# Kernel tuning notes

Measured on AMD Instinct MI355X. Metric: run time of the kernel, lower is better.

Reference implementation:

```python
import jax, jax.numpy as jnp
import numpy as np

B, T, F, U = 64, 512, 1024, 64


def setup_inputs() -> dict:
    key = jax.random.key(0)
    ks = jax.random.split(key, 6)
    return {
        "x": jax.random.normal(ks[0], (B, T, F), dtype=jnp.float32),
        "kernel": jax.random.normal(ks[1], (F, U), dtype=jnp.float32) * (1.0 / np.sqrt(F)),
        "bias": jax.random.normal(ks[2], (U,), dtype=jnp.float32) * 0.02,
        "chain_kernel": jax.random.normal(ks[3], (U, U), dtype=jnp.float32) * 0.1,
        "left_boundary": jax.random.normal(ks[4], (U,), dtype=jnp.float32) * 0.1,
        "right_boundary": jax.random.normal(ks[5], (U,), dtype=jnp.float32) * 0.1,
    }


def _viterbi_decode(potentials, chain_kernel):
    # potentials: [B, T, U], chain_kernel: [U, U]
    def step(alpha, pot_t):
        # alpha: [B, U] best score ending in each tag at t-1
        scores = alpha[:, :, None] + chain_kernel[None, :, :] + pot_t[:, None, :]  # [B, U_prev, U_cur]
        return jnp.max(scores, axis=1), jnp.argmax(scores, axis=1)

    pots_t = jnp.moveaxis(potentials[:, 1:], 1, 0)  # [T-1, B, U]
    alpha_last, backptrs = jax.lax.scan(step, potentials[:, 0], pots_t)
    last_tag = jnp.argmax(alpha_last, axis=-1)  # [B]

    def back(tag, bp):
        prev = jnp.take_along_axis(bp, tag[:, None], axis=1)[:, 0]
        return prev, prev

    _, tags = jax.lax.scan(back, last_tag, backptrs, reverse=True)  # [T-1, B], positions 0..T-2
    path = jnp.concatenate([jnp.moveaxis(tags, 0, 1), last_tag[:, None]], axis=1)
    return path.astype(jnp.int32)


def reference(x, kernel, bias, chain_kernel, left_boundary, right_boundary):
    # dense projection (activation = linear)
    potentials = jnp.einsum("btf,fu->btu", x, kernel) + bias  # [B, T, U]
    # boundary energies (mask=None path: add to first/last timestep)
    potentials = potentials.at[:, 0, :].add(left_boundary)
    potentials = potentials.at[:, -1, :].add(right_boundary)
    return _viterbi_decode(potentials, chain_kernel)
```

## Files before the change

### kernel.cpp

```cpp
#include <hip/hip_runtime.h>

#define B_ 64
#define T_ 512
#define F_ 1024
#define U_ 64

__global__ __launch_bounds__(256) void crf_gemm_kernel(
    const float* __restrict__ x, const float* __restrict__ w,
    const float* __restrict__ bias, const float* __restrict__ lb,
    const float* __restrict__ rb, float* __restrict__ pot)
{
    const int tid = threadIdx.x;
    const int rt = tid >> 4;
    const int ut = tid & 15;
    const int n0 = blockIdx.x * 128;
    const int r0 = rt * 8;
    const int u0 = ut * 4;

    float acc[8][4];
#pragma unroll
    for (int i = 0; i < 8; ++i)
#pragma unroll
        for (int j = 0; j < 4; ++j) acc[i][j] = 0.f;

    const float* xbase = x + (size_t)(n0 + r0) * F_;

    for (int f4 = 0; f4 < F_ / 4; ++f4) {
        float xv[8][4];
#pragma unroll
        for (int i = 0; i < 8; ++i) {
            const float4 t4 = *reinterpret_cast<const float4*>(
                xbase + (size_t)i * F_ + f4 * 4);
            xv[i][0] = t4.x; xv[i][1] = t4.y; xv[i][2] = t4.z; xv[i][3] = t4.w;
        }
        float kv[4][4];
#pragma unroll
        for (int ff = 0; ff < 4; ++ff) {
            const float4 t4 = *reinterpret_cast<const float4*>(
                w + (size_t)(f4 * 4 + ff) * U_ + u0);
            kv[ff][0] = t4.x; kv[ff][1] = t4.y; kv[ff][2] = t4.z; kv[ff][3] = t4.w;
        }
#pragma unroll
        for (int ff = 0; ff < 4; ++ff)
#pragma unroll
            for (int i = 0; i < 8; ++i)
#pragma unroll
                for (int j = 0; j < 4; ++j)
                    acc[i][j] = fmaf(xv[i][ff], kv[ff][j], acc[i][j]);
    }

    const int t0 = n0 & (T_ - 1);
    const float4 bs4 = *reinterpret_cast<const float4*>(bias + u0);
    const float4 lb4 = *reinterpret_cast<const float4*>(lb + u0);
    const float4 rb4 = *reinterpret_cast<const float4*>(rb + u0);

#pragma unroll
    for (int i = 0; i < 8; ++i) {
        const int n = n0 + r0 + i;
        const int t = t0 + r0 + i;
        float4 o;
        o.x = acc[i][0] + bs4.x;
        o.y = acc[i][1] + bs4.y;
        o.z = acc[i][2] + bs4.z;
        o.w = acc[i][3] + bs4.w;
        if (t == 0)      { o.x += lb4.x; o.y += lb4.y; o.z += lb4.z; o.w += lb4.w; }
        if (t == T_ - 1) { o.x += rb4.x; o.y += rb4.y; o.z += rb4.z; o.w += rb4.w; }
        *reinterpret_cast<float4*>(pot + (size_t)n * U_ + u0) = o;
    }
}

__global__ __launch_bounds__(256) void crf_viterbi_kernel(
    const float* __restrict__ pot, const float* __restrict__ chain,
    int* __restrict__ path)
{
    const int b = blockIdx.x;
    const int tid = threadIdx.x;
    const int u = tid & 63;
    const int g = tid >> 6;

    __shared__ __align__(16) float alpha_s[64];
    __shared__ float pval[4][64];
    __shared__ int   pidx[4][64];
    __shared__ unsigned char bp[T_ - 1][64];

    float chain_r[16];
#pragma unroll
    for (int k = 0; k < 16; ++k)
        chain_r[k] = chain[(size_t)(g * 16 + k) * U_ + u];

    const float* potb = pot + (size_t)b * T_ * U_;

    if (g == 0) alpha_s[u] = potb[u];
    __syncthreads();

    float pc = potb[(size_t)U_ + u];

    for (int t = 1; t < T_; ++t) {
        const int tn = (t + 1 < T_) ? (t + 1) : (T_ - 1);
        const float pn = potb[(size_t)tn * U_ + u];

        const float4* a4 = reinterpret_cast<const float4*>(alpha_s);
        float best = -3.402823466e38f;
        int bidx = 0;
#pragma unroll
        for (int q = 0; q < 4; ++q) {
            const float4 av = a4[g * 4 + q];
            const float avv[4] = {av.x, av.y, av.z, av.w};
#pragma unroll
            for (int kk = 0; kk < 4; ++kk) {
                const int k = q * 4 + kk;
                const float s2 = (avv[kk] + chain_r[k]) + pc;
                if (s2 > best) { best = s2; bidx = g * 16 + k; }
            }
        }
        pval[g][u] = best;
        pidx[g][u] = bidx;
        __syncthreads();
        if (g == 0) {
            float bv = pval[0][u];
            int   bi = pidx[0][u];
#pragma unroll
            for (int j = 1; j < 4; ++j) {
                const float v = pval[j][u];
                if (v > bv) { bv = v; bi = pidx[j][u]; }
            }
            bp[t - 1][u] = (unsigned char)bi;
            alpha_s[u] = bv;
        }
        __syncthreads();
        pc = pn;
    }

    if (tid == 0) {
        float bv = alpha_s[0];
        int bi = 0;
        for (int v = 1; v < 64; ++v) {
            const float a = alpha_s[v];
            if (a > bv) { bv = a; bi = v; }
        }
        int* pb = path + (size_t)b * T_;
        int tag = bi;
        pb[T_ - 1] = tag;
        for (int t = T_ - 2; t >= 0; --t) {
            tag = bp[t][tag];
            pb[t] = tag;
        }
    }
}

extern "C" void kernel_launch(void* const* d_in, const int* in_sizes, int n_in,
                              void* d_out, int out_size, void* d_ws, size_t ws_size,
                              hipStream_t stream) {
    const float* x  = (const float*)d_in[0];
    const float* w  = (const float*)d_in[1];
    const float* bs = (const float*)d_in[2];
    const float* ck = (const float*)d_in[3];
    const float* lb = (const float*)d_in[4];
    const float* rb = (const float*)d_in[5];

    float* pot = (float*)d_ws;
    int* path  = (int*)d_out;

    crf_gemm_kernel<<<dim3(256), dim3(256), 0, stream>>>(x, w, bs, lb, rb, pot);
    crf_viterbi_kernel<<<dim3(B_), dim3(256), 0, stream>>>(pot, ck, path);
}
```

Baseline: 414.9 us.

## Shrink GEMM tiles for more blocks and parallelize Viterbi backtrace across wavefronts

```diff
diff --git a/kernel.cpp b/kernel.cpp
--- a/kernel.cpp
+++ b/kernel.cpp
@@ -5,7 +5,7 @@
 #define F_ 1024
 #define U_ 64
 
-__global__ __launch_bounds__(256) void crf_gemm_kernel(
+__global__ __launch_bounds__(256, 4) void crf_gemm_kernel(
     const float* __restrict__ x, const float* __restrict__ w,
     const float* __restrict__ bias, const float* __restrict__ lb,
     const float* __restrict__ rb, float* __restrict__ pot)
@@ -13,40 +13,41 @@
     const int tid = threadIdx.x;
     const int rt = tid >> 4;
     const int ut = tid & 15;
-    const int n0 = blockIdx.x * 128;
-    const int r0 = rt * 8;
+    const int n0 = blockIdx.x * 32;
+    const int r0 = rt * 2;
     const int u0 = ut * 4;
 
-    float acc[8][4];
-#pragma unroll
-    for (int i = 0; i < 8; ++i)
-#pragma unroll
-        for (int j = 0; j < 4; ++j) acc[i][j] = 0.f;
-
-    const float* xbase = x + (size_t)(n0 + r0) * F_;
-
-    for (int f4 = 0; f4 < F_ / 4; ++f4) {
-        float xv[8][4];
-#pragma unroll
-        for (int i = 0; i < 8; ++i) {
-            const float4 t4 = *reinterpret_cast<const float4*>(
-                xbase + (size_t)i * F_ + f4 * 4);
-            xv[i][0] = t4.x; xv[i][1] = t4.y; xv[i][2] = t4.z; xv[i][3] = t4.w;
-        }
-        float kv[4][4];
-#pragma unroll
-        for (int ff = 0; ff < 4; ++ff) {
-            const float4 t4 = *reinterpret_cast<const float4*>(
-                w + (size_t)(f4 * 4 + ff) * U_ + u0);
-            kv[ff][0] = t4.x; kv[ff][1] = t4.y; kv[ff][2] = t4.z; kv[ff][3] = t4.w;
-        }
-#pragma unroll
-        for (int ff = 0; ff < 4; ++ff)
-#pragma unroll
-            for (int i = 0; i < 8; ++i)
-#pragma unroll
-                for (int j = 0; j < 4; ++j)
-                    acc[i][j] = fmaf(xv[i][ff], kv[ff][j], acc[i][j]);
+    float acc0[4] = {0.f, 0.f, 0.f, 0.f};
+    float acc1[4] = {0.f, 0.f, 0.f, 0.f};
+
+    const float* xp = x + (size_t)(n0 + r0) * F_;
+    const float* wp = w + u0;
+
+    for (int it = 0; it < F_ / 8; ++it) {
+        const float4 xa0 = *reinterpret_cast<const float4*>(xp);
+        const float4 xb0 = *reinterpret_cast<const float4*>(xp + 4);
+        const float4 xa1 = *reinterpret_cast<const float4*>(xp + F_);
+        const float4 xb1 = *reinterpret_cast<const float4*>(xp + F_ + 4);
+        float4 kv[8];
+#pragma unroll
+        for (int ff = 0; ff < 8; ++ff)
+            kv[ff] = *reinterpret_cast<const float4*>(wp + ff * U_);
+
+        const float xr0[8] = {xa0.x, xa0.y, xa0.z, xa0.w, xb0.x, xb0.y, xb0.z, xb0.w};
+        const float xr1[8] = {xa1.x, xa1.y, xa1.z, xa1.w, xb1.x, xb1.y, xb1.z, xb1.w};
+#pragma unroll
+        for (int ff = 0; ff < 8; ++ff) {
+            acc0[0] = fmaf(xr0[ff], kv[ff].x, acc0[0]);
+            acc0[1] = fmaf(xr0[ff], kv[ff].y, acc0[1]);
+            acc0[2] = fmaf(xr0[ff], kv[ff].z, acc0[2]);
+            acc0[3] = fmaf(xr0[ff], kv[ff].w, acc0[3]);
+            acc1[0] = fmaf(xr1[ff], kv[ff].x, acc1[0]);
+            acc1[1] = fmaf(xr1[ff], kv[ff].y, acc1[1]);
+            acc1[2] = fmaf(xr1[ff], kv[ff].z, acc1[2]);
+            acc1[3] = fmaf(xr1[ff], kv[ff].w, acc1[3]);
+        }
+        xp += 8;
+        wp += 8 * U_;
     }
 
     const int t0 = n0 & (T_ - 1);
@@ -55,14 +56,15 @@
     const float4 rb4 = *reinterpret_cast<const float4*>(rb + u0);
 
 #pragma unroll
-    for (int i = 0; i < 8; ++i) {
+    for (int i = 0; i < 2; ++i) {
+        const float* a = (i == 0) ? acc0 : acc1;
         const int n = n0 + r0 + i;
         const int t = t0 + r0 + i;
         float4 o;
-        o.x = acc[i][0] + bs4.x;
-        o.y = acc[i][1] + bs4.y;
-        o.z = acc[i][2] + bs4.z;
-        o.w = acc[i][3] + bs4.w;
+        o.x = a[0] + bs4.x;
+        o.y = a[1] + bs4.y;
+        o.z = a[2] + bs4.z;
+        o.w = a[3] + bs4.w;
         if (t == 0)      { o.x += lb4.x; o.y += lb4.y; o.z += lb4.z; o.w += lb4.w; }
         if (t == T_ - 1) { o.x += rb4.x; o.y += rb4.y; o.z += rb4.z; o.w += rb4.w; }
         *reinterpret_cast<float4*>(pot + (size_t)n * U_ + u0) = o;
@@ -82,6 +84,9 @@
     __shared__ float pval[4][64];
     __shared__ int   pidx[4][64];
     __shared__ unsigned char bp[T_ - 1][64];
+    __shared__ int cmap[4][64];
+    __shared__ int es[4];
+    __shared__ int last_s;
 
     float chain_r[16];
 #pragma unroll
@@ -93,57 +98,98 @@
     if (g == 0) alpha_s[u] = potb[u];
     __syncthreads();
 
-    float pc = potb[(size_t)U_ + u];
+    float pc = potb[U_ + u];
+    int C = u;
+    const int r0c = g * 128;
+    const int r1c = (g == 3) ? (T_ - 1) : (g + 1) * 128;
 
     for (int t = 1; t < T_; ++t) {
         const int tn = (t + 1 < T_) ? (t + 1) : (T_ - 1);
         const float pn = potb[(size_t)tn * U_ + u];
 
         const float4* a4 = reinterpret_cast<const float4*>(alpha_s);
-        float best = -3.402823466e38f;
-        int bidx = 0;
+        float s[16];
 #pragma unroll
         for (int q = 0; q < 4; ++q) {
             const float4 av = a4[g * 4 + q];
-            const float avv[4] = {av.x, av.y, av.z, av.w};
-#pragma unroll
-            for (int kk = 0; kk < 4; ++kk) {
-                const int k = q * 4 + kk;
-                const float s2 = (avv[kk] + chain_r[k]) + pc;
-                if (s2 > best) { best = s2; bidx = g * 16 + k; }
-            }
-        }
-        pval[g][u] = best;
-        pidx[g][u] = bidx;
+            s[q * 4 + 0] = (av.x + chain_r[q * 4 + 0]) + pc;
+            s[q * 4 + 1] = (av.y + chain_r[q * 4 + 1]) + pc;
+            s[q * 4 + 2] = (av.z + chain_r[q * 4 + 2]) + pc;
+            s[q * 4 + 3] = (av.w + chain_r[q * 4 + 3]) + pc;
+        }
+        float tv[8]; int ti[8];
+#pragma unroll
+        for (int i = 0; i < 8; ++i) {
+            const bool gt = s[2 * i + 1] > s[2 * i];
+            tv[i] = gt ? s[2 * i + 1] : s[2 * i];
+            ti[i] = gt ? 2 * i + 1 : 2 * i;
+        }
+        float uv[4]; int ui[4];
+#pragma unroll
+        for (int i = 0; i < 4; ++i) {
+            const bool gt = tv[2 * i + 1] > tv[2 * i];
+            uv[i] = gt ? tv[2 * i + 1] : tv[2 * i];
+            ui[i] = gt ? ti[2 * i + 1] : ti[2 * i];
+        }
+        const bool gw0 = uv[1] > uv[0];
+        const float wv0 = gw0 ? uv[1] : uv[0];
+        const int   wi0 = gw0 ? ui[1] : ui[0];
+        const bool gw1 = uv[3] > uv[2];
+        const float wv1 = gw1 ? uv[3] : uv[2];
+        const int   wi1 = gw1 ? ui[3] : ui[2];
+        const bool gf = wv1 > wv0;
+        const float bv16 = gf ? wv1 : wv0;
+        const int   bi16 = gf ? wi1 : wi0;
+
+        pval[g][u] = bv16;
+        pidx[g][u] = g * 16 + bi16;
         __syncthreads();
+
+        const float p0 = pval[0][u], p1 = pval[1][u];
+        const float p2 = pval[2][u], p3 = pval[3][u];
+        const int   j0 = pidx[0][u], j1 = pidx[1][u];
+        const int   j2 = pidx[2][u], j3 = pidx[3][u];
+        const bool ga = p1 > p0; const float va = ga ? p1 : p0; const int ia = ga ? j1 : j0;
+        const bool gb = p3 > p2; const float vb = gb ? p3 : p2; const int ib = gb ? j3 : j2;
+        const bool gc = vb > va; const float bv = gc ? vb : va; const int bi = gc ? ib : ia;
+
         if (g == 0) {
-            float bv = pval[0][u];
-            int   bi = pidx[0][u];
-#pragma unroll
-            for (int j = 1; j < 4; ++j) {
-                const float v = pval[j][u];
-                if (v > bv) { bv = v; bi = pidx[j][u]; }
-            }
+            alpha_s[u] = bv;
             bp[t - 1][u] = (unsigned char)bi;
-            alpha_s[u] = bv;
-        }
+        }
+        const int r = t - 1;
+        if (r >= r0c && r < r1c)
+            C = __builtin_amdgcn_ds_bpermute(bi << 2, C);
         __syncthreads();
         pc = pn;
     }
 
+    cmap[g][u] = C;
     if (tid == 0) {
-        float bv = alpha_s[0];
-        int bi = 0;
+        float bvv = alpha_s[0];
+        int bii = 0;
         for (int v = 1; v < 64; ++v) {
             const float a = alpha_s[v];
-            if (a > bv) { bv = a; bi = v; }
-        }
+            if (a > bvv) { bvv = a; bii = v; }
+        }
+        last_s = bii;
+        path[(size_t)b * T_ + (T_ - 1)] = bii;
+    }
+    __syncthreads();
+    if (tid == 0) {
+        const int e3 = last_s;
+        const int e2 = cmap[3][e3];
+        const int e1 = cmap[2][e2];
+        const int e0 = cmap[1][e1];
+        es[0] = e0; es[1] = e1; es[2] = e2; es[3] = e3;
+    }
+    __syncthreads();
+    if (u == 0) {
+        int tag = es[g];
         int* pb = path + (size_t)b * T_;
-        int tag = bi;
-        pb[T_ - 1] = tag;
-        for (int t = T_ - 2; t >= 0; --t) {
-            tag = bp[t][tag];
-            pb[t] = tag;
+        for (int r = r1c - 1; r >= r0c; --r) {
+            tag = bp[r][tag];
+            pb[r] = tag;
         }
     }
 }
@@ -161,6 +207,6 @@
     float* pot = (float*)d_ws;
     int* path  = (int*)d_out;
 
-    crf_gemm_kernel<<<dim3(256), dim3(256), 0, stream>>>(x, w, bs, lb, rb, pot);
+    crf_gemm_kernel<<<dim3(B_ * T_ / 32), dim3(256), 0, stream>>>(x, w, bs, lb, rb, pot);
     crf_viterbi_kernel<<<dim3(B_), dim3(256), 0, stream>>>(pot, ck, path);
 }
```

New measurement: 488.7 us. 17.8% more time.
